# Kernel tuning notes

Hardware: AMD Instinct MI355X
Metric: run time of the kernel (lower is better)

Reference implementation:

```python
import jax, jax.numpy as jnp
import numpy as np
from jax import lax

DIM = 256
HEADS = 8
DIM_HEAD = 64
INNER = HEADS * DIM_HEAD  # 512
K = 3
PAD = K // 2
KV_STRIDE = 2
SCALE = DIM_HEAD ** -0.5
BN_EPS = 1e-5


def _dw_block(x, w_dw, g, b, m, v, w_pw, stride):
    """depthwise conv -> batchnorm (eval) -> 1x1 conv. x: [B,C,H,W]."""
    c = x.shape[1]
    h = lax.conv_general_dilated(
        x, w_dw, window_strides=(stride, stride),
        padding=[(PAD, PAD), (PAD, PAD)],
        feature_group_count=c,
        dimension_numbers=('NCHW', 'OIHW', 'NCHW'))
    inv = lax.rsqrt(v + BN_EPS)
    h = (h - m[None, :, None, None]) * (g * inv)[None, :, None, None] + b[None, :, None, None]
    return jnp.einsum('oc,bchw->bohw', w_pw, h)


def _heads_flat(t):
    # [B, h*d, H, W] -> [B, h, d, H*W]
    B, hd, H, W = t.shape
    return t.reshape(B, HEADS, DIM_HEAD, H * W)


def _cross_attn(q, k, v, Hq, Wq):
    # q: [B,h,d,i], k/v: [B,h,d,j]
    dots = jnp.einsum('bhdi,bhdj->bhij', q, k) * SCALE
    attn = jax.nn.softmax(dots, axis=-1)
    out = jnp.einsum('bhij,bhdj->bhdi', attn, v)
    B = q.shape[0]
    return out.reshape(B, INNER, Hq, Wq)


def _forward(x, y, q_dw_w, q_bn_gamma, q_bn_beta, q_bn_mean, q_bn_var, q_pw_w,
             kv_dw_w, kv_bn_gamma, kv_bn_beta, kv_bn_mean, kv_bn_var, kv_pw_w,
             out_w, out_b):
    B, _, Hx, Wx = x.shape
    _, _, Hy, Wy = y.shape

    qx = _heads_flat(_dw_block(x, q_dw_w, q_bn_gamma, q_bn_beta, q_bn_mean, q_bn_var, q_pw_w, 1))
    kvx = _dw_block(x, kv_dw_w, kv_bn_gamma, kv_bn_beta, kv_bn_mean, kv_bn_var, kv_pw_w, KV_STRIDE)
    kx, vx = map(_heads_flat, jnp.split(kvx, 2, axis=1))

    qy = _heads_flat(_dw_block(y, q_dw_w, q_bn_gamma, q_bn_beta, q_bn_mean, q_bn_var, q_pw_w, 1))
    kvy = _dw_block(y, kv_dw_w, kv_bn_gamma, kv_bn_beta, kv_bn_mean, kv_bn_var, kv_pw_w, KV_STRIDE)
    ky, vy = map(_heads_flat, jnp.split(kvy, 2, axis=1))

    outx = _cross_attn(qx, ky, vy, Hx, Wx)   # x queries attend to y keys/values
    outy = _cross_attn(qy, kx, vx, Hy, Wy)   # y queries attend to x keys/values

    def proj(o):
        return jnp.einsum('oc,bchw->bohw', out_w, o) + out_b[None, :, None, None]

    return proj(outx), proj(outy)


def setup_inputs() -> dict:
    key = jax.random.key(0)
    ks = jax.random.split(key, 8)
    B, H, W = 8, 32, 32
    return {
        'x': jax.random.normal(ks[0], (B, DIM, H, W), jnp.float32),
        'y': jax.random.normal(ks[1], (B, DIM, H, W), jnp.float32),
        'q_dw_w': jax.random.normal(ks[2], (DIM, 1, K, K), jnp.float32) * 0.1,
        'q_bn_gamma': jnp.ones((DIM,), jnp.float32),
        'q_bn_beta': jnp.zeros((DIM,), jnp.float32),
        'q_bn_mean': jnp.zeros((DIM,), jnp.float32),
        'q_bn_var': jnp.ones((DIM,), jnp.float32),
        'q_pw_w': jax.random.normal(ks[3], (INNER, DIM), jnp.float32) * (DIM ** -0.5),
        'kv_dw_w': jax.random.normal(ks[4], (DIM, 1, K, K), jnp.float32) * 0.1,
        'kv_bn_gamma': jnp.ones((DIM,), jnp.float32),
        'kv_bn_beta': jnp.zeros((DIM,), jnp.float32),
        'kv_bn_mean': jnp.zeros((DIM,), jnp.float32),
        'kv_bn_var': jnp.ones((DIM,), jnp.float32),
        'kv_pw_w': jax.random.normal(ks[5], (2 * INNER, DIM), jnp.float32) * (DIM ** -0.5),
        'out_w': jax.random.normal(ks[6], (DIM, INNER), jnp.float32) * (INNER ** -0.5),
        'out_b': jnp.zeros((DIM,), jnp.float32),
    }


def reference(x, y, q_dw_w, q_bn_gamma, q_bn_beta, q_bn_mean, q_bn_var, q_pw_w,
              kv_dw_w, kv_bn_gamma, kv_bn_beta, kv_bn_mean, kv_bn_var, kv_pw_w,
              out_w, out_b):
    return _forward(x, y, q_dw_w, q_bn_gamma, q_bn_beta, q_bn_mean, q_bn_var, q_pw_w,
                    kv_dw_w, kv_bn_gamma, kv_bn_beta, kv_bn_mean, kv_bn_var, kv_pw_w,
                    out_w, out_b)
```

## Files before the change

### kernel.cpp

```cpp
#include <hip/hip_runtime.h>

#define BN_EPS 1e-5f
#define ATT_SCALE 0.125f

typedef _Float16 half_t;
typedef _Float16 half8 __attribute__((ext_vector_type(8)));
typedef _Float16 half4 __attribute__((ext_vector_type(4)));
typedef float f32x4 __attribute__((ext_vector_type(4)));

__device__ __forceinline__ void gll16(const void* g, void* l) {
    __builtin_amdgcn_global_load_lds((const __attribute__((address_space(1))) void*)g,
                                     (__attribute__((address_space(3))) void*)l, 16, 0, 0);
}

__device__ void prep_body(
    int o, int c,
    const float* qg, const float* qb, const float* qm, const float* qv, const float* qpw,
    const float* kg, const float* kbt, const float* km, const float* kvv, const float* kvpw,
    const float* outw,
    half_t* wq, half_t* wkv, half_t* wout, float* bq, float* bkv, float* red)
{
    if (o >= 1536) {
        int ro = o - 1536;
        #pragma unroll
        for (int ci = 0; ci < 2; ++ci) {
            int cc = ci * 256 + c;
            float wv = outw[(size_t)ro * 512 + cc];
            half_t hh = (half_t)wv;
            wout[(size_t)ro * 1024 + cc]       = hh;
            wout[(size_t)ro * 1024 + 512 + cc] = (half_t)(wv - (float)hh);
        }
        return;
    }
    const float *g, *b, *m, *v, *w; half_t* we; float* be;
    if (o < 512) {
        g = qg; b = qb; m = qm; v = qv;
        w = qpw + (size_t)o * 256; we = wq + (size_t)o * 512; be = bq + o;
    } else {
        int ro = o - 512;
        g = kg; b = kbt; m = km; v = kvv;
        w = kvpw + (size_t)ro * 256; we = wkv + (size_t)ro * 512; be = bkv + ro;
    }
    float s  = g[c] * rsqrtf(v[c] + BN_EPS);
    float tt = b[c] - m[c] * s;
    float wv = w[c];
    float wsv = wv * s;
    half_t hh = (half_t)wsv;
    we[c]       = hh;
    we[256 + c] = (half_t)(wsv - (float)hh);
    float partial = wv * tt;
    #pragma unroll
    for (int off = 32; off > 0; off >>= 1)
        partial += __shfl_down(partial, off, 64);
    if ((c & 63) == 0) red[c >> 6] = partial;
    __syncthreads();
    if (c == 0) *be = red[0] + red[1] + red[2] + red[3];
}

__device__ void dw_body(
    int rp, int img, float* sin,
    const float* x, const float* y,
    const float* qdw, const float* kvdw,
    half_t* qB, half_t* kvB)
{
    const float* in = (img < 8) ? x + (size_t)img * 256 * 1024
// ... 37 lines not shown
            #pragma unroll
            for (int c8 = 0; c8 < 8; ++c8) {
                float acc = 0.f;
                #pragma unroll
                for (int dr = 0; dr < 3; ++dr)
                    #pragma unroll
                    for (int dc = 0; dc < 3; ++dc)
                        acc += wq9[dr * 3 + dc] * rowv[r + dr][c8 + dc + 1];
                half_t hh = (half_t)acc;
                size_t p = (size_t)img * 1024 + (2 * rp + r) * 32 + cg * 8 + c8;
                qB[p * 512 + gch]       = hh;
                qB[p * 512 + 256 + gch] = (half_t)(acc - (float)hh);
            }
        }
        #pragma unroll
        for (int c4 = 0; c4 < 4; ++c4) {
            float acc = 0.f;
            #pragma unroll
            for (int dr = 0; dr < 3; ++dr)
                #pragma unroll
                for (int dc = 0; dc < 3; ++dc)
                    acc += wk9[dr * 3 + dc] * rowv[dr][2 * c4 + dc + 1];
            half_t hh = (half_t)acc;
            size_t p = (size_t)img * 256 + rp * 16 + cg * 4 + c4;
            kvB[p * 512 + gch]       = hh;
            kvB[p * 512 + 256 + gch] = (half_t)(acc - (float)hh);
        }
    }
}

__global__ __launch_bounds__(256) void prep_dw_kernel(
    const float* __restrict__ x, const float* __restrict__ y,
    const float* __restrict__ qdw, const float* __restrict__ kvdw,
    const float* __restrict__ qg, const float* __restrict__ qb,
    const float* __restrict__ qm, const float* __restrict__ qv,
    const float* __restrict__ qpw,
    const float* __restrict__ kg, const float* __restrict__ kbt,
    const float* __restrict__ km, const float* __restrict__ kvv,
    const float* __restrict__ kvpw,
    const float* __restrict__ outw,
    half_t* __restrict__ wq, half_t* __restrict__ wkv, half_t* __restrict__ wout,
    float* __restrict__ bq, float* __restrict__ bkv,
    half_t* __restrict__ qB, half_t* __restrict__ kvB)
{
    __shared__ __align__(16) float smem[64 * 148];
    int bx = blockIdx.x;
    if (bx < 256)
        dw_body(bx & 15, bx >> 4, smem, x, y, qdw, kvdw, qB, kvB);
    else
        prep_body(bx - 256, threadIdx.x, qg, qb, qm, qv, qpw,
                  kg, kbt, km, kvv, kvpw, outw, wq, wkv, wout, bq, bkv, smem);
}

template<int MT, int NT, int WGM, int WGN, int NTHR, int MODE>
__device__ __forceinline__ void gemm_worker(
    char* lds, const half_t* Ab, const half_t* Bb,
    void* outBuf, const float* bias,
    int K, int NPX, int img, int m0, int n0, float scale)
{
    constexpr int TM = WGM * MT * 16, TN = WGN * NT * 16;
    constexpr int BUF = (TM + TN) * 128;
    int t = threadIdx.x, w = t >> 6, lane = t & 63, quad = lane >> 4, l15 = lane & 15;
    int wm = w % WGM, wn = w / WGM;
    f32x4 acc[MT][NT] = {};
    const int NC = K / 32;

    auto stage = [&](int kh, int p) {
        char* Ah = lds + p * BUF;
        char* Al = Ah + TM * 64;
        char* Bh = Ah + TM * 128;
        char* Bl = Bh + TN * 64;
        #pragma unroll
        for (int ii = 0; ii < TM * 4 / NTHR; ++ii) {
            int u = ii * NTHR + t;
            int mt = u >> 6, q = (u >> 4) & 3, r = u & 15;
            const half_t* g = Ab + (size_t)(mt * 16 + r) * (2 * K) + kh + q * 8;
            gll16(g,     Ah + (u & ~63) * 16);
            gll16(g + K, Al + (u & ~63) * 16);
        }
        #pragma unroll
        for (int ii = 0; ii < TN * 4 / NTHR; ++ii) {
            int u = ii * NTHR + t;
            int nt = u >> 6, q = (u >> 4) & 3, r = u & 15;
            const half_t* g = Bb + (size_t)(nt * 16 + r) * (2 * K) + kh + q * 8;
            gll16(g,     Bh + (u & ~63) * 16);
            gll16(g + K, Bl + (u & ~63) * 16);
        }
    };

    stage(0, 0);
    for (int kc = 0; kc < NC; ++kc) {
        __syncthreads();
        if (kc + 1 < NC) stage((kc + 1) * 32, (kc + 1) & 1);
        char* Ah = lds + (kc & 1) * BUF;
        char* Al = Ah + TM * 64;
        char* Bh = Ah + TM * 128;
        char* Bl = Bh + TN * 64;
        half8 afh[MT], afl[MT];
        #pragma unroll
        for (int mi = 0; mi < MT; ++mi) {
            afh[mi] = *(half8*)(Ah + (wm * MT + mi) * 1024 + lane * 16);
            afl[mi] = *(half8*)(Al + (wm * MT + mi) * 1024 + lane * 16);
        }
        #pragma unroll
        for (int ni = 0; ni < NT; ++ni) {
            half8 bh = *(half8*)(Bh + (wn * NT + ni) * 1024 + lane * 16);
            half8 bl = *(half8*)(Bl + (wn * NT + ni) * 1024 + lane * 16);
            #pragma unroll
            for (int mi = 0; mi < MT; ++mi) {
                acc[mi][ni] = __builtin_amdgcn_mfma_f32_16x16x32_f16(afh[mi], bh, acc[mi][ni], 0, 0, 0);
                acc[mi][ni] = __builtin_amdgcn_mfma_f32_16x16x32_f16(afh[mi], bl, acc[mi][ni], 0, 0, 0);
                acc[mi][ni] = __builtin_amdgcn_mfma_f32_16x16x32_f16(afl[mi], bh, acc[mi][ni], 0, 0, 0);
            }
        }
    }

    if (MODE == 2) {
        #pragma unroll
        for (int mi = 0; mi < MT; ++mi) {
            int mrow0 = m0 + wm * MT * 16 + mi * 16 + quad * 4;
            #pragma unroll
            for (int ni = 0; ni < NT; ++ni) {
                int col = n0 + wn * NT * 16 + ni * 16 + l15;
                f32x4 a = acc[mi][ni];
                float* op = (float*)outBuf + (size_t)img * 256 * NPX;
                #pragma unroll
                for (int r = 0; r < 4; ++r)
                    op[(size_t)(mrow0 + r) * NPX + col] = a[r] + bias[mrow0 + r];
            }
        }
    } else {
        __syncthreads();
        float* tbuf = (float*)lds;
        constexpr int TP = 40;
        #pragma unroll
        for (int qtr = 0; qtr < TM / 32; ++qtr) {
            #pragma unroll
            for (int mi = 0; mi < MT; ++mi) {
                int rowblk = wm * MT * 16 + mi * 16;
                if (rowblk >= qtr * 32 && rowblk < qtr * 32 + 32) {
                    int mloc = rowblk - qtr * 32 + quad * 4;
                    #pragma unroll
                    for (int ni = 0; ni < NT; ++ni) {
                        int nloc = wn * NT * 16 + ni * 16 + l15;
                        #pragma unroll
                        for (int r = 0; r < 4; ++r) {
                            float vv = acc[mi][ni][r];
                            if (MODE == 0) vv = (vv + bias[m0 + rowblk + quad * 4 + r]) * scale;
                            else           vv = vv + bias[n0 + nloc];
                            tbuf[nloc * TP + mloc + r] = vv;
                        }
                    }
                }
            }
            __syncthreads();
            #pragma unroll
            for (int it = 0; it < (TN * 4) / NTHR; ++it) {
                int u = it * NTHR + t;
                int n = u >> 2, mg = u & 3;
                float vv[8];
                *(float4*)&vv[0] = *(const float4*)&tbuf[n * TP + mg * 8];
                *(float4*)&vv[4] = *(const float4*)&tbuf[n * TP + mg * 8 + 4];
                half8 hv, lv;
                #pragma unroll
                for (int j = 0; j < 8; ++j) {
                    half_t hh = (half_t)vv[j];
                    hv[j] = hh; lv[j] = (half_t)(vv[j] - (float)hh);
                }
                int mglob = m0 + qtr * 32 + mg * 8;
                if (MODE == 0) {
                    int h = mglob >> 6, d0 = mglob & 63;
                    half_t* op = (half_t*)outBuf + ((size_t)(img * 8 + h) * NPX + n0 + n) * 128 + d0;
                    *(half8*)op = hv;
                    *(half8*)(op + 64) = lv;
                } else {
                    int nn = n0 + n, h = nn >> 6, d = nn & 63;
                    int j0 = mglob;
                    half_t* op = (half_t*)outBuf + (size_t)(img * 8 + h) * 32768
                               + (j0 >> 5) * 4096 + ((d >> 4) & 3) * 512 + ((j0 >> 4) & 1) * 256
                               + ((j0 >> 2) & 3) * 64 + (d & 15) * 4;
                    half4 a0 = {hv[0], hv[1], hv[2], hv[3]};
                    half4 a1 = {hv[4], hv[5], hv[6], hv[7]};
                    half4 b0 = {lv[0], lv[1], lv[2], lv[3]};
                    half4 b1 = {lv[4], lv[5], lv[6], lv[7]};
                    *(half4*)op               = a0;
                    *(half4*)(op + 64)        = a1;
                    *(half4*)(op + 2048)      = b0;
                    *(half4*)(op + 2048 + 64) = b1;
                }
            }
            __syncthreads();
        }
    }
}

__global__ __launch_bounds__(512, 4) void qkv_kernel(
    const half_t* __restrict__ wq, const half_t* __restrict__ wkv,
    const half_t* __restrict__ qB, const half_t* __restrict__ kvB,
    const float* __restrict__ bq, const float* __restrict__ bkv,
    half_t* __restrict__ qpr, half_t* __restrict__ kpr, half_t* __restrict__ vpr)
{
    __shared__ __align__(16) char lds[65536];
    int tile = blockIdx.x, img = blockIdx.z;
    if (tile < 32) {
        int m0 = (tile >> 3) * 128, n0 = (tile & 7) * 128;
        gemm_worker<2, 4, 4, 2, 512, 0>(lds,
            wq + (size_t)m0 * 512,
            qB + (size_t)img * (1024 * 512) + (size_t)n0 * 512,
            qpr, bq, 256, 1024, img, m0, n0, ATT_SCALE);
    } else if (tile < 40) {
        int tt = tile - 32;
        int m0 = (tt >> 1) * 128, n0 = (tt & 1) * 128;
        gemm_worker<2, 4, 4, 2, 512, 0>(lds,
            wkv + (size_t)m0 * 512,
            kvB + (size_t)img * (256 * 512) + (size_t)n0 * 512,
            kpr, bkv, 256, 256, img, m0, n0, 1.0f);
    } else {
        int tt = tile - 40;
        int m0 = (tt >> 2) * 128, n0 = (tt & 3) * 128;
        gemm_worker<2, 4, 4, 2, 512, 1>(lds,
            kvB + (size_t)img * (256 * 512) + (size_t)m0 * 512,
            wkv + (size_t)(512 + n0) * 512,
            vpr, bkv + 512, 256, 512, img, m0, n0, 1.0f);
    }
}

__global__ __launch_bounds__(256, 3) void out_kernel(
    const half_t* __restrict__ wout, const half_t* __restrict__ attp,
    const float* __restrict__ outb, float* __restrict__ out)
{
    __shared__ __align__(16) char lds[49152];
    int tile = blockIdx.x, img = blockIdx.z;
    int m0 = (tile >> 3) * 64, n0 = (tile & 7) * 128;
    gemm_worker<2, 4, 2, 2, 256, 2>(lds,
        wout + (size_t)m0 * 1024,
        attp + (size_t)img * (1024 * 1024) + (size_t)n0 * 1024,
        out, outb, 512, 1024, img, m0, n0, 1.0f);
}

__global__ __launch_bounds__(256, 4) void attn_fused(
    const half_t* __restrict__ qb, const half_t* __restrict__ kb,
    const half_t* __restrict__ vb, half_t* __restrict__ att)
{
    __shared__ __align__(16) char lds[17408];
    int ic2 = blockIdx.y;
    int img = blockIdx.x & 15, h = blockIdx.x >> 4;
    int partner = img ^ 8;
    int t = threadIdx.x, w = t >> 6, lane = t & 63, quad = lane >> 4, l15 = lane & 15;
    const half_t* qp = qb + ((size_t)(img * 8 + h) * 1024 + ic2 * 64) * 128;
    const half_t* kp = kb + (size_t)(partner * 8 + h) * 256 * 128;
    const half_t* vp = vb + (size_t)(partner * 8 + h) * 32768;

    half8 qh[2], ql[2];
    #pragma unroll
    for (int kcs = 0; kcs < 2; ++kcs) {
        const half_t* qr = qp + (size_t)(w * 16 + l15) * 128 + kcs * 32 + quad * 8;
        qh[kcs] = *(const half8*)qr;
        ql[kcs] = *(const half8*)(qr + 64);
    }

    auto stageK = [&](int c, char* buf) {
        #pragma unroll
        for (int s = 0; s < 2; ++s) {
            int u = s * 256 + t;
            int sb = u >> 6, li = u & 63;
            int plane = sb >> 2, ntr = (sb >> 1) & 1, kcs = sb & 1;
            const half_t* g = kp + (size_t)(c * 32 + ntr * 16 + (li & 15)) * 128
                                 + plane * 64 + kcs * 32 + (li >> 4) * 8;
            gll16(g, buf + (u & ~63) * 16);
        }
    };
    auto stageV = [&](int c, char* buf) {
        #pragma unroll
        for (int s = 0; s < 2; ++s) {
            int u = s * 256 + t;
            gll16(vp + (size_t)c * 4096 + u * 8, buf + (u & ~63) * 16);
        }
    };

    f32x4 sacc[16] = {};
    stageK(0, lds);
    #pragma unroll
    for (int c = 0; c < 8; ++c) {
        __syncthreads();
        char* nb = lds + (((c + 1) & 1) * 8192);
        if (c < 7) stageK(c + 1, nb); else stageV(0, nb);
        const char* buf = lds + ((c & 1) * 8192);
        __builtin_amdgcn_s_setprio(1);
        #pragma unroll
        for (int kcs = 0; kcs < 2; ++kcs)
            #pragma unroll
            for (int ntr = 0; ntr < 2; ++ntr) {
                half8 kh = *(const half8*)(buf + (ntr * 2 + kcs) * 1024 + lane * 16);
                half8 kl = *(const half8*)(buf + 4096 + (ntr * 2 + kcs) * 1024 + lane * 16);
                f32x4 s = sacc[c * 2 + ntr];
                s = __builtin_amdgcn_mfma_f32_16x16x32_f16(kh, qh[kcs], s, 0, 0, 0);
                s = __builtin_amdgcn_mfma_f32_16x16x32_f16(kh, ql[kcs], s, 0, 0, 0);
                s = __builtin_amdgcn_mfma_f32_16x16x32_f16(kl, qh[kcs], s, 0, 0, 0);
                sacc[c * 2 + ntr] = s;
            }
        __builtin_amdgcn_s_setprio(0);
    }

    float mx = sacc[0][0];
    #pragma unroll
    for (int ti = 0; ti < 16; ++ti)
        #pragma unroll
        for (int r = 0; r < 4; ++r) mx = fmaxf(mx, sacc[ti][r]);
    mx = fmaxf(mx, __shfl_xor(mx, 16, 64));
    mx = fmaxf(mx, __shfl_xor(mx, 32, 64));

    f32x4 oacc[4] = {};
    float lsum = 0.f;
    #pragma unroll
    for (int c = 0; c < 8; ++c) {
        half4 pb[2][2];
        #pragma unroll
        for (int kk = 0; kk < 2; ++kk) {
            f32x4 s = sacc[c * 2 + kk];
            #pragma unroll
            for (int e = 0; e < 4; ++e) {
                float pv = __expf(s[e] - mx);
                lsum += pv;
                half_t hh = (half_t)pv;
                pb[kk][0][e] = hh;
                pb[kk][1][e] = (half_t)(pv - (float)hh);
            }
        }
        __syncthreads();
        if (c < 7) stageV(c + 1, lds + (((c + 1) & 1) * 8192));
        const char* buf = lds + ((c & 1) * 8192);
        __builtin_amdgcn_s_setprio(1);
        #pragma unroll
        for (int mt = 0; mt < 4; ++mt) {
            #pragma unroll
            for (int kk = 0; kk < 2; ++kk) {
                half4 vh = *(const half4*)(buf + (mt * 2 + kk) * 512 + lane * 8);
                half4 vl = *(const half4*)(buf + 4096 + (mt * 2 + kk) * 512 + lane * 8);
                f32x4 o = oacc[mt];
                o = __builtin_amdgcn_mfma_f32_16x16x16f16(vh, pb[kk][0], o, 0, 0, 0);
                o = __builtin_amdgcn_mfma_f32_16x16x16f16(vh, pb[kk][1], o, 0, 0, 0);
                o = __builtin_amdgcn_mfma_f32_16x16x16f16(vl, pb[kk][0], o, 0, 0, 0);
                oacc[mt] = o;
            }
        }
        __builtin_amdgcn_s_setprio(0);
    }

    lsum += __shfl_xor(lsum, 16, 64);
    lsum += __shfl_xor(lsum, 32, 64);
    float inv = 1.f / lsum;

    __syncthreads();
    #pragma unroll
    for (int mt = 0; mt < 4; ++mt)
        #pragma unroll
        for (int r = 0; r < 4; ++r) {
            float vv = oacc[mt][r] * inv;
            half_t hh = (half_t)vv;
            int row = w * 16 + l15;
            int d = mt * 16 + quad * 4 + r;
            *(half_t*)(lds + (row * 132 + d) * 2)      = hh;
            *(half_t*)(lds + (row * 132 + 64 + d) * 2) = (half_t)(vv - (float)hh);
        }
    __syncthreads();
    #pragma unroll
    for (int ii = 0; ii < 4; ++ii) {
        int u = ii * 256 + t;
        int i = u >> 4, s16 = u & 15;
        half8 val = *(const half8*)(lds + (i * 132 + (s16 >> 3) * 64 + (s16 & 7) * 8) * 2);
        *(half8*)(att + ((size_t)img * 1024 + ic2 * 64 + i) * 1024
                  + (s16 >> 3) * 512 + h * 64 + (s16 & 7) * 8) = val;
    }
}

extern "C" void kernel_launch(void* const* d_in, const int* in_sizes, int n_in,
                              void* d_out, int out_size, void* d_ws, size_t ws_size,
                              hipStream_t stream) {
    const float* x    = (const float*)d_in[0];
    const float* y    = (const float*)d_in[1];
    const float* qdw  = (const float*)d_in[2];
    const float* qg   = (const float*)d_in[3];
    const float* qbb  = (const float*)d_in[4];
    const float* qm   = (const float*)d_in[5];
    const float* qv   = (const float*)d_in[6];
    const float* qpw  = (const float*)d_in[7];
    const float* kvdw = (const float*)d_in[8];
    const float* kg   = (const float*)d_in[9];
    const float* kb_  = (const float*)d_in[10];
    const float* km   = (const float*)d_in[11];
    const float* kvv  = (const float*)d_in[12];
    const float* kvpw = (const float*)d_in[13];
    const float* outw = (const float*)d_in[14];
    const float* outb = (const float*)d_in[15];

    char* ws = (char*)d_ws;
    half_t* wq   = (half_t*)(ws);
    half_t* wkv  = (half_t*)(ws + 524288);
    half_t* wout = (half_t*)(ws + 1572864);
    float*  bq   = (float*) (ws + 2097152);
    float*  bkv  = (float*) (ws + 2099200);
    half_t* qpr  = (half_t*)(ws + 2103296);
    half_t* kpr  = (half_t*)(ws + 35657728);
    half_t* vpr  = (half_t*)(ws + 44046336);
    half_t* qB   = (half_t*)(ws + 52434944);
    half_t* kvB  = (half_t*)(ws + 69212160);
    half_t* attp = (half_t*)(ws + 52434944);

    prep_dw_kernel<<<2048, 256, 0, stream>>>(
        x, y, qdw, kvdw, qg, qbb, qm, qv, qpw, kg, kb_, km, kvv, kvpw, outw,
        wq, wkv, wout, bq, bkv, qB, kvB);

    qkv_kernel<<<dim3(48, 1, 16), 512, 0, stream>>>(
        wq, wkv, qB, kvB, bq, bkv, qpr, kpr, vpr);

    attn_fused<<<dim3(128, 16, 1), 256, 0, stream>>>(qpr, kpr, vpr, attp);

    out_kernel<<<dim3(32, 1, 16), 256, 0, stream>>>(wout, attp, outb, (float*)d_out);
}
```

Baseline: 213.3 us.

## Use 256x256 register-staged QKV tiles and deeper-pipelined 128-query attention blocks

Measured after the change: 219.0 us. +2.7%, slower.

```diff
diff --git a/kernel.cpp b/kernel.cpp
--- a/kernel.cpp
+++ b/kernel.cpp
@@ -11,6 +11,11 @@
 __device__ __forceinline__ void gll16(const void* g, void* l) {
     __builtin_amdgcn_global_load_lds((const __attribute__((address_space(1))) void*)g,
                                      (__attribute__((address_space(3))) void*)l, 16, 0, 0);
+}
+
+template<int N>
+__device__ __forceinline__ void vmwait() {
+    asm volatile("s_waitcnt vmcnt(%0)" :: "i"(N) : "memory");
 }
 
 __device__ void prep_body(
@@ -154,6 +159,172 @@
                   kg, kbt, km, kvv, kvpw, outw, wq, wkv, wout, bq, bkv, smem);
 }
 
+template<int MODE>
+__device__ void gemm_sq(char* lds, const half_t* Ab, const half_t* Bb,
+                        void* outBuf, const float* bias,
+                        int NPX, int img, int m0, int n0, float scale)
+{
+    int t = threadIdx.x, w = t >> 6, lane = t & 63, quad = lane >> 4, l15 = lane & 15;
+    int wm = w & 3, wn = w >> 2;
+    f32x4 acc[4][4] = {};
+
+    const int side = t >> 9, pl = (t >> 8) & 1, r = t & 255;
+    const half_t* gsrc = (side ? Bb : Ab) + (size_t)r * 512 + pl * 256;
+    char* ldst = lds + side * 32768 + pl * 16384 + r * 16;
+
+    half8 greg[4];
+    #pragma unroll
+    for (int q = 0; q < 4; ++q) greg[q] = *(const half8*)(gsrc + q * 8);
+
+    for (int kc = 0; kc < 8; ++kc) {
+        __syncthreads();
+        #pragma unroll
+        for (int q = 0; q < 4; ++q) *(half8*)(ldst + q * 4096) = greg[q];
+        __syncthreads();
+        if (kc < 7) {
+            const half_t* gs2 = gsrc + (kc + 1) * 32;
+            #pragma unroll
+            for (int q = 0; q < 4; ++q) greg[q] = *(const half8*)(gs2 + q * 8);
+        }
+        #pragma unroll
+        for (int mh = 0; mh < 2; ++mh) {
+            half8 mfh[2], mfl[2];
+            #pragma unroll
+            for (int mi2 = 0; mi2 < 2; ++mi2) {
+                int mrow = (wm * 4 + mh * 2 + mi2) * 16 + l15;
+                mfh[mi2] = *(const half8*)(lds + quad * 4096 + mrow * 16);
+                mfl[mi2] = *(const half8*)(lds + 16384 + quad * 4096 + mrow * 16);
+            }
+            #pragma unroll
+            for (int ni = 0; ni < 4; ++ni) {
+                int nrow = (wn * 4 + ni) * 16 + l15;
+                half8 nh = *(const half8*)(lds + 32768 + quad * 4096 + nrow * 16);
+                half8 nl = *(const half8*)(lds + 49152 + quad * 4096 + nrow * 16);
+                #pragma unroll
+                for (int mi2 = 0; mi2 < 2; ++mi2) {
+                    int mi = mh * 2 + mi2;
+                    acc[mi][ni] = __builtin_amdgcn_mfma_f32_16x16x32_f16(mfh[mi2], nh, acc[mi][ni], 0, 0, 0);
+                    acc[mi][ni] = __builtin_amdgcn_mfma_f32_16x16x32_f16(mfh[mi2], nl, acc[mi][ni], 0, 0, 0);
+                    acc[mi][ni] = __builtin_amdgcn_mfma_f32_16x16x32_f16(mfl[mi2], nh, acc[mi][ni], 0, 0, 0);
+                }
+            }
+        }
+    }
+
+    if (MODE == 0) {
+        float* tbuf = (float*)lds;
+        #pragma unroll
+        for (int rr = 0; rr < 8; ++rr) {
+            __syncthreads();
+            if (wm == (rr >> 1)) {
+                #pragma unroll
+                for (int mi2 = 0; mi2 < 2; ++mi2) {
+                    int mi = (rr & 1) * 2 + mi2;
+                    #pragma unroll
+                    for (int ni = 0; ni < 4; ++ni)
+                        #pragma unroll
+                        for (int r4 = 0; r4 < 4; ++r4) {
+                            float vv = (acc[mi][ni][r4]
+                                        + bias[m0 + rr * 32 + mi2 * 16 + quad * 4 + r4]) * scale;
+                            tbuf[(wn * 64 + ni * 16 + l15) * 36 + mi2 * 16 + quad * 4 + r4] = vv;
+                        }
+                }
+            }
+            __syncthreads();
+            {
+                int n = t >> 2, mg = t & 3;
+                float vv[8];
+                *(float4*)&vv[0] = *(const float4*)&tbuf[n * 36 + mg * 8];
+                *(float4*)&vv[4] = *(const float4*)&tbuf[n * 36 + mg * 8 + 4];
+                half8 hv, lv;
+                #pragma unroll
+                for (int j = 0; j < 8; ++j) {
+                    half_t hh = (half_t)vv[j];
+                    hv[j] = hh; lv[j] = (half_t)(vv[j] - (float)hh);
+                }
+                int mglob = m0 + rr * 32 + mg * 8;
+                int h = mglob >> 6, d0 = mglob & 63;
+                half_t* op = (half_t*)outBuf + ((size_t)(img * 8 + h) * NPX + n0 + n) * 128 + d0;
+                *(half8*)op = hv;
+                *(half8*)(op + 64) = lv;
+            }
+        }
+    } else {
+        float* tbuf = (float*)lds;
+        constexpr int TP = 40;
+        #pragma unroll
+        for (int qtr = 0; qtr < 8; ++qtr) {
+            __syncthreads();
+            if (wm == (qtr >> 1)) {
+                #pragma unroll
+                for (int mi2 = 0; mi2 < 2; ++mi2) {
+                    int mi = (qtr & 1) * 2 + mi2;
+                    #pragma unroll
+                    for (int ni = 0; ni < 4; ++ni) {
+                        int nloc = wn * 64 + ni * 16 + l15;
+                        #pragma unroll
+                        for (int r4 = 0; r4 < 4; ++r4)
+                            tbuf[nloc * TP + mi2 * 16 + quad * 4 + r4] =
+                                acc[mi][ni][r4] + bias[n0 + nloc];
+                    }
+                }
+            }
+            __syncthreads();
+            {
+                int n = t >> 2, mg = t & 3;
+                float vv[8];
+                *(float4*)&vv[0] = *(const float4*)&tbuf[n * TP + mg * 8];
+                *(float4*)&vv[4] = *(const float4*)&tbuf[n * TP + mg * 8 + 4];
+                half8 hv, lv;
+                #pragma unroll
+                for (int j = 0; j < 8; ++j) {
+                    half_t hh = (half_t)vv[j];
+                    hv[j] = hh; lv[j] = (half_t)(vv[j] - (float)hh);
+                }
+                int j0 = qtr * 32 + mg * 8;
+                int nn = n0 + n, h = nn >> 6, d = nn & 63;
+                half_t* op = (half_t*)outBuf + (size_t)(img * 8 + h) * 32768
+                           + (j0 >> 5) * 4096 + ((d >> 4) & 3) * 512 + ((j0 >> 4) & 1) * 256
+                           + ((j0 >> 2) & 3) * 64 + (d & 15) * 4;
+                half4 a0 = {hv[0], hv[1], hv[2], hv[3]};
+                half4 a1 = {hv[4], hv[5], hv[6], hv[7]};
+                half4 b0 = {lv[0], lv[1], lv[2], lv[3]};
+                half4 b1 = {lv[4], lv[5], lv[6], lv[7]};
+                *(half4*)op               = a0;
+                *(half4*)(op + 64)        = a1;
+                *(half4*)(op + 2048)      = b0;
+                *(half4*)(op + 2048 + 64) = b1;
+            }
+        }
+    }
+}
+
+__global__ __launch_bounds__(1024, 4) void qkv_kernel(
+    const half_t* __restrict__ wq, const half_t* __restrict__ wkv,
+    const half_t* __restrict__ qB, const half_t* __restrict__ kvB,
+    const float* __restrict__ bq, const float* __restrict__ bkv,
+    half_t* __restrict__ qpr, half_t* __restrict__ kpr, half_t* __restrict__ vpr)
+{
+    __shared__ __align__(16) char lds[65536];
+    int tile = blockIdx.x, img = blockIdx.z;
+    if (tile < 8) {
+        int m0 = (tile >> 2) * 256, n0 = (tile & 3) * 256;
+        gemm_sq<0>(lds, wq + (size_t)m0 * 512,
+                   qB + (size_t)img * (1024 * 512) + (size_t)n0 * 512,
+                   qpr, bq, 1024, img, m0, n0, ATT_SCALE);
+    } else if (tile < 10) {
+        int m0 = (tile - 8) * 256;
+        gemm_sq<0>(lds, wkv + (size_t)m0 * 512,
+                   kvB + (size_t)img * (256 * 512),
+                   kpr, bkv, 256, img, m0, 0, 1.0f);
+    } else {
+        int n0 = (tile - 10) * 256;
+        gemm_sq<1>(lds, kvB + (size_t)img * (256 * 512),
+                   wkv + (size_t)(512 + n0) * 512,
+                   vpr, bkv + 512, 512, img, 0, n0, 1.0f);
+    }
+}
+
 template<int MT, int NT, int WGM, int WGN, int NTHR, int MODE>
 __device__ __forceinline__ void gemm_worker(
     char* lds, const half_t* Ab, const half_t* Bb,
@@ -175,16 +346,16 @@
         #pragma unroll
         for (int ii = 0; ii < TM * 4 / NTHR; ++ii) {
             int u = ii * NTHR + t;
-            int mt = u >> 6, q = (u >> 4) & 3, r = u & 15;
-            const half_t* g = Ab + (size_t)(mt * 16 + r) * (2 * K) + kh + q * 8;
+            int mt = u >> 6, q = (u >> 4) & 3, rr = u & 15;
+            const half_t* g = Ab + (size_t)(mt * 16 + rr) * (2 * K) + kh + q * 8;
             gll16(g,     Ah + (u & ~63) * 16);
             gll16(g + K, Al + (u & ~63) * 16);
         }
         #pragma unroll
         for (int ii = 0; ii < TN * 4 / NTHR; ++ii) {
             int u = ii * NTHR + t;
-            int nt = u >> 6, q = (u >> 4) & 3, r = u & 15;
-            const half_t* g = Bb + (size_t)(nt * 16 + r) * (2 * K) + kh + q * 8;
+            int nt = u >> 6, q = (u >> 4) & 3, rr = u & 15;
+            const half_t* g = Bb + (size_t)(nt * 16 + rr) * (2 * K) + kh + q * 8;
             gll16(g,     Bh + (u & ~63) * 16);
             gll16(g + K, Bl + (u & ~63) * 16);
         }
@@ -217,113 +388,18 @@
         }
     }
 
-    if (MODE == 2) {
-        #pragma unroll
-        for (int mi = 0; mi < MT; ++mi) {
-            int mrow0 = m0 + wm * MT * 16 + mi * 16 + quad * 4;
-            #pragma unroll
-            for (int ni = 0; ni < NT; ++ni) {
-                int col = n0 + wn * NT * 16 + ni * 16 + l15;
-                f32x4 a = acc[mi][ni];
-                float* op = (float*)outBuf + (size_t)img * 256 * NPX;
-                #pragma unroll
-                for (int r = 0; r < 4; ++r)
-                    op[(size_t)(mrow0 + r) * NPX + col] = a[r] + bias[mrow0 + r];
-            }
-        }
-    } else {
-        __syncthreads();
-        float* tbuf = (float*)lds;
-        constexpr int TP = 40;
-        #pragma unroll
-        for (int qtr = 0; qtr < TM / 32; ++qtr) {
-            #pragma unroll
-            for (int mi = 0; mi < MT; ++mi) {
-                int rowblk = wm * MT * 16 + mi * 16;
-                if (rowblk >= qtr * 32 && rowblk < qtr * 32 + 32) {
-                    int mloc = rowblk - qtr * 32 + quad * 4;
-                    #pragma unroll
-                    for (int ni = 0; ni < NT; ++ni) {
-                        int nloc = wn * NT * 16 + ni * 16 + l15;
-                        #pragma unroll
-                        for (int r = 0; r < 4; ++r) {
-                            float vv = acc[mi][ni][r];
-                            if (MODE == 0) vv = (vv + bias[m0 + rowblk + quad * 4 + r]) * scale;
-                            else           vv = vv + bias[n0 + nloc];
-                            tbuf[nloc * TP + mloc + r] = vv;
-                        }
-                    }
-                }
-            }
-            __syncthreads();
-            #pragma unroll
-            for (int it = 0; it < (TN * 4) / NTHR; ++it) {
-                int u = it * NTHR + t;
-                int n = u >> 2, mg = u & 3;
-                float vv[8];
-                *(float4*)&vv[0] = *(const float4*)&tbuf[n * TP + mg * 8];
-                *(float4*)&vv[4] = *(const float4*)&tbuf[n * TP + mg * 8 + 4];
-                half8 hv, lv;
-                #pragma unroll
-                for (int j = 0; j < 8; ++j) {
-                    half_t hh = (half_t)vv[j];
-                    hv[j] = hh; lv[j] = (half_t)(vv[j] - (float)hh);
-                }
-                int mglob = m0 + qtr * 32 + mg * 8;
-                if (MODE == 0) {
-                    int h = mglob >> 6, d0 = mglob & 63;
-                    half_t* op = (half_t*)outBuf + ((size_t)(img * 8 + h) * NPX + n0 + n) * 128 + d0;
-                    *(half8*)op = hv;
-                    *(half8*)(op + 64) = lv;
-                } else {
-                    int nn = n0 + n, h = nn >> 6, d = nn & 63;
-                    int j0 = mglob;
-                    half_t* op = (half_t*)outBuf + (size_t)(img * 8 + h) * 32768
-                               + (j0 >> 5) * 4096 + ((d >> 4) & 3) * 512 + ((j0 >> 4) & 1) * 256
-                               + ((j0 >> 2) & 3) * 64 + (d & 15) * 4;
-                    half4 a0 = {hv[0], hv[1], hv[2], hv[3]};
-                    half4 a1 = {hv[4], hv[5], hv[6], hv[7]};
-                    half4 b0 = {lv[0], lv[1], lv[2], lv[3]};
-                    half4 b1 = {lv[4], lv[5], lv[6], lv[7]};
-                    *(half4*)op               = a0;
-                    *(half4*)(op + 64)        = a1;
-                    *(half4*)(op + 2048)      = b0;
-                    *(half4*)(op + 2048 + 64) = b1;
-                }
-            }
-            __syncthreads();
-        }
-    }
-}
-
-__global__ __launch_bounds__(512, 4) void qkv_kernel(
-    const half_t* __restrict__ wq, const half_t* __restrict__ wkv,
-    const half_t* __restrict__ qB, const half_t* __restrict__ kvB,
-    const float* __restrict__ bq, const float* __restrict__ bkv,
-    half_t* __restrict__ qpr, half_t* __restrict__ kpr, half_t* __restrict__ vpr)
-{
-    __shared__ __align__(16) char lds[65536];
-    int tile = blockIdx.x, img = blockIdx.z;
-    if (tile < 32) {
-        int m0 = (tile >> 3) * 128, n0 = (tile & 7) * 128;
-        gemm_worker<2, 4, 4, 2, 512, 0>(lds,
-            wq + (size_t)m0 * 512,
-            qB + (size_t)img * (1024 * 512) + (size_t)n0 * 512,
-            qpr, bq, 256, 1024, img, m0, n0, ATT_SCALE);
-    } else if (tile < 40) {
-        int tt = tile - 32;
-        int m0 = (tt >> 1) * 128, n0 = (tt & 1) * 128;
-        gemm_worker<2, 4, 4, 2, 512, 0>(lds,
-            wkv + (size_t)m0 * 512,
-            kvB + (size_t)img * (256 * 512) + (size_t)n0 * 512,
-            kpr, bkv, 256, 256, img, m0, n0, 1.0f);
-    } else {
-        int tt = tile - 40;
-        int m0 = (tt >> 2) * 128, n0 = (tt & 3) * 128;
-        gemm_worker<2, 4, 4, 2, 512, 1>(lds,
-            kvB + (size_t)img * (256 * 512) + (size_t)m0 * 512,
-            wkv + (size_t)(512 + n0) * 512,
-            vpr, bkv + 512, 256, 512, img, m0, n0, 1.0f);
+    #pragma unroll
+    for (int mi = 0; mi < MT; ++mi) {
+        int mrow0 = m0 + wm * MT * 16 + mi * 16 + quad * 4;
+        #pragma unroll
+        for (int ni = 0; ni < NT; ++ni) {
+            int col = n0 + wn * NT * 16 + ni * 16 + l15;
+            f32x4 a = acc[mi][ni];
+            float* op = (float*)outBuf + (size_t)img * 256 * NPX;
+            #pragma unroll
+            for (int rr = 0; rr < 4; ++rr)
+                op[(size_t)(mrow0 + rr) * NPX + col] = a[rr] + bias[mrow0 + rr];
+        }
     }
 }
 
@@ -340,16 +416,16 @@
         out, outb, 512, 1024, img, m0, n0, 1.0f);
 }
 
-__global__ __launch_bounds__(256, 4) void attn_fused(
+__global__ __launch_bounds__(512, 4) void attn_fused(
     const half_t* __restrict__ qb, const half_t* __restrict__ kb,
     const half_t* __restrict__ vb, half_t* __restrict__ att)
 {
-    __shared__ __align__(16) char lds[17408];
-    int ic2 = blockIdx.y;
+    __shared__ __align__(16) char lds[33792];
+    int ic = blockIdx.y;
     int img = blockIdx.x & 15, h = blockIdx.x >> 4;
     int partner = img ^ 8;
     int t = threadIdx.x, w = t >> 6, lane = t & 63, quad = lane >> 4, l15 = lane & 15;
-    const half_t* qp = qb + ((size_t)(img * 8 + h) * 1024 + ic2 * 64) * 128;
+    const half_t* qp = qb + ((size_t)(img * 8 + h) * 1024 + ic * 128) * 128;
     const half_t* kp = kb + (size_t)(partner * 8 + h) * 256 * 128;
     const half_t* vp = vb + (size_t)(partner * 8 + h) * 32768;
 
@@ -361,92 +437,89 @@
         ql[kcs] = *(const half8*)(qr + 64);
     }
 
-    auto stageK = [&](int c, char* buf) {
-        #pragma unroll
-        for (int s = 0; s < 2; ++s) {
-            int u = s * 256 + t;
-            int sb = u >> 6, li = u & 63;
+    auto stageC = [&](int c) {
+        char* buf = lds + (c & 3) * 8192;
+        if (c < 8) {
+            int sb = t >> 6, li = t & 63;
             int plane = sb >> 2, ntr = (sb >> 1) & 1, kcs = sb & 1;
             const half_t* g = kp + (size_t)(c * 32 + ntr * 16 + (li & 15)) * 128
                                  + plane * 64 + kcs * 32 + (li >> 4) * 8;
-            gll16(g, buf + (u & ~63) * 16);
+            gll16(g, buf + (t & ~63) * 16);
+        } else {
+            gll16(vp + (size_t)(c - 8) * 4096 + t * 8, buf + (t & ~63) * 16);
         }
     };
-    auto stageV = [&](int c, char* buf) {
-        #pragma unroll
-        for (int s = 0; s < 2; ++s) {
-            int u = s * 256 + t;
-            gll16(vp + (size_t)c * 4096 + u * 8, buf + (u & ~63) * 16);
-        }
-    };
 
     f32x4 sacc[16] = {};
-    stageK(0, lds);
-    #pragma unroll
-    for (int c = 0; c < 8; ++c) {
-        __syncthreads();
-        char* nb = lds + (((c + 1) & 1) * 8192);
-        if (c < 7) stageK(c + 1, nb); else stageV(0, nb);
-        const char* buf = lds + ((c & 1) * 8192);
-        __builtin_amdgcn_s_setprio(1);
-        #pragma unroll
-        for (int kcs = 0; kcs < 2; ++kcs)
-            #pragma unroll
-            for (int ntr = 0; ntr < 2; ++ntr) {
-                half8 kh = *(const half8*)(buf + (ntr * 2 + kcs) * 1024 + lane * 16);
-                half8 kl = *(const half8*)(buf + 4096 + (ntr * 2 + kcs) * 1024 + lane * 16);
-                f32x4 s = sacc[c * 2 + ntr];
-                s = __builtin_amdgcn_mfma_f32_16x16x32_f16(kh, qh[kcs], s, 0, 0, 0);
-                s = __builtin_amdgcn_mfma_f32_16x16x32_f16(kh, ql[kcs], s, 0, 0, 0);
-                s = __builtin_amdgcn_mfma_f32_16x16x32_f16(kl, qh[kcs], s, 0, 0, 0);
-                sacc[c * 2 + ntr] = s;
-            }
-        __builtin_amdgcn_s_setprio(0);
-    }
-
-    float mx = sacc[0][0];
-    #pragma unroll
-    for (int ti = 0; ti < 16; ++ti)
-        #pragma unroll
-        for (int r = 0; r < 4; ++r) mx = fmaxf(mx, sacc[ti][r]);
-    mx = fmaxf(mx, __shfl_xor(mx, 16, 64));
-    mx = fmaxf(mx, __shfl_xor(mx, 32, 64));
-
     f32x4 oacc[4] = {};
-    float lsum = 0.f;
-    #pragma unroll
-    for (int c = 0; c < 8; ++c) {
-        half4 pb[2][2];
-        #pragma unroll
-        for (int kk = 0; kk < 2; ++kk) {
-            f32x4 s = sacc[c * 2 + kk];
-            #pragma unroll
-            for (int e = 0; e < 4; ++e) {
-                float pv = __expf(s[e] - mx);
-                lsum += pv;
-                half_t hh = (half_t)pv;
-                pb[kk][0][e] = hh;
-                pb[kk][1][e] = (half_t)(pv - (float)hh);
-            }
-        }
-        __syncthreads();
-        if (c < 7) stageV(c + 1, lds + (((c + 1) & 1) * 8192));
-        const char* buf = lds + ((c & 1) * 8192);
-        __builtin_amdgcn_s_setprio(1);
-        #pragma unroll
-        for (int mt = 0; mt < 4; ++mt) {
+    float mx = 0.f, lsum = 0.f;
+
+    stageC(0); stageC(1); stageC(2);
+
+    #pragma unroll
+    for (int c = 0; c < 16; ++c) {
+        if (c < 14)       vmwait<2>();
+        else if (c == 14) vmwait<1>();
+        else              vmwait<0>();
+        __builtin_amdgcn_s_barrier();
+        __builtin_amdgcn_sched_barrier(0);
+        if (c + 3 < 16) stageC(c + 3);
+        const char* buf = lds + (c & 3) * 8192;
+        if (c < 8) {
+            __builtin_amdgcn_s_setprio(1);
+            #pragma unroll
+            for (int kcs = 0; kcs < 2; ++kcs)
+                #pragma unroll
+                for (int ntr = 0; ntr < 2; ++ntr) {
+                    half8 kh = *(const half8*)(buf + (ntr * 2 + kcs) * 1024 + lane * 16);
+                    half8 kl = *(const half8*)(buf + 4096 + (ntr * 2 + kcs) * 1024 + lane * 16);
+                    f32x4 s = sacc[c * 2 + ntr];
+                    s = __builtin_amdgcn_mfma_f32_16x16x32_f16(kh, qh[kcs], s, 0, 0, 0);
+                    s = __builtin_amdgcn_mfma_f32_16x16x32_f16(kh, ql[kcs], s, 0, 0, 0);
+                    s = __builtin_amdgcn_mfma_f32_16x16x32_f16(kl, qh[kcs], s, 0, 0, 0);
+                    sacc[c * 2 + ntr] = s;
+                }
+            __builtin_amdgcn_s_setprio(0);
+        } else {
+            if (c == 8) {
+                float m_ = sacc[0][0];
+                #pragma unroll
+                for (int ti = 0; ti < 16; ++ti)
+                    #pragma unroll
+                    for (int r = 0; r < 4; ++r) m_ = fmaxf(m_, sacc[ti][r]);
+                m_ = fmaxf(m_, __shfl_xor(m_, 16, 64));
+                mx = fmaxf(m_, __shfl_xor(m_, 32, 64));
+            }
+            int jc = c - 8;
+            half4 pb[2][2];
             #pragma unroll
             for (int kk = 0; kk < 2; ++kk) {
-                half4 vh = *(const half4*)(buf + (mt * 2 + kk) * 512 + lane * 8);
-                half4 vl = *(const half4*)(buf + 4096 + (mt * 2 + kk) * 512 + lane * 8);
-                f32x4 o = oacc[mt];
-                o = __builtin_amdgcn_mfma_f32_16x16x16f16(vh, pb[kk][0], o, 0, 0, 0);
-                o = __builtin_amdgcn_mfma_f32_16x16x16f16(vh, pb[kk][1], o, 0, 0, 0);
-                o = __builtin_amdgcn_mfma_f32_16x16x16f16(vl, pb[kk][0], o, 0, 0, 0);
-                oacc[mt] = o;
-            }
-        }
-        __builtin_amdgcn_s_setprio(0);
+                f32x4 s = sacc[jc * 2 + kk];
+                #pragma unroll
+                for (int e = 0; e < 4; ++e) {
+                    float pv = __expf(s[e] - mx);
+                    lsum += pv;
+                    half_t hh = (half_t)pv;
+                    pb[kk][0][e] = hh;
+                    pb[kk][1][e] = (half_t)(pv - (float)hh);
+                }
+            }
+            __builtin_amdgcn_s_setprio(1);
+            #pragma unroll
+            for (int mt = 0; mt < 4; ++mt) {
+                #pragma unroll
+                for (int kk = 0; kk < 2; ++kk) {
+                    half4 vh = *(const half4*)(buf + (mt * 2 + kk) * 512 + lane * 8);
+                    half4 vl = *(const half4*)(buf + 4096 + (mt * 2 + kk) * 512 + lane * 8);
+                    f32x4 o = oacc[mt];
+                    o = __builtin_amdgcn_mfma_f32_16x16x16f16(vh, pb[kk][0], o, 0, 0, 0);
+                    o = __builtin_amdgcn_mfma_f32_16x16x16f16(vh, pb[kk][1], o, 0, 0, 0);
+                    o = __builtin_amdgcn_mfma_f32_16x16x16f16(vl, pb[kk][0], o, 0, 0, 0);
+                    oacc[mt] = o;
+                }
+            }
+            __builtin_amdgcn_s_setprio(0);
+        }
     }
 
     lsum += __shfl_xor(lsum, 16, 64);
@@ -468,11 +541,11 @@
     __syncthreads();
     #pragma unroll
     for (int ii = 0; ii < 4; ++ii) {
-        int u = ii * 256 + t;
-        int i = u >> 4, s16 = u & 15;
-        half8 val = *(const half8*)(lds + (i * 132 + (s16 >> 3) * 64 + (s16 & 7) * 8) * 2);
-        *(half8*)(att + ((size_t)img * 1024 + ic2 * 64 + i) * 1024
-                  + (s16 >> 3) * 512 + h * 64 + (s16 & 7) * 8) = val;
+        int u = ii * 512 + t;
+        int i = u >> 4, seg = (u >> 3) & 1, p8 = u & 7;
+        half8 val = *(const half8*)(lds + (i * 132 + seg * 64 + p8 * 8) * 2);
+        *(half8*)(att + ((size_t)img * 1024 + ic * 128 + i) * 1024
+                  + seg * 512 + h * 64 + p8 * 8) = val;
     }
 }
 
@@ -513,10 +586,10 @@
         x, y, qdw, kvdw, qg, qbb, qm, qv, qpw, kg, kb_, km, kvv, kvpw, outw,
         wq, wkv, wout, bq, bkv, qB, kvB);
 
-    qkv_kernel<<<dim3(48, 1, 16), 512, 0, stream>>>(
+    qkv_kernel<<<dim3(12, 1, 16), 1024, 0, stream>>>(
         wq, wkv, qB, kvB, bq, bkv, qpr, kpr, vpr);
 
-    attn_fused<<<dim3(128, 16, 1), 256, 0, stream>>>(qpr, kpr, vpr, attp);
+    attn_fused<<<dim3(128, 8, 1), 512, 0, stream>>>(qpr, kpr, vpr, attp);
 
     out_kernel<<<dim3(32, 1, 16), 256, 0, stream>>>(wout, attp, outb, (float*)d_out);
 }
```

## Deepen attention pipeline, widen blocks, and use vmcnt-based barriers in GEMM

Applied to the files above, without the earlier changes.

Result: faster. 204.0 us (-4.4%).

```diff
diff --git a/kernel.cpp b/kernel.cpp
--- a/kernel.cpp
+++ b/kernel.cpp
@@ -11,6 +11,11 @@
 __device__ __forceinline__ void gll16(const void* g, void* l) {
     __builtin_amdgcn_global_load_lds((const __attribute__((address_space(1))) void*)g,
                                      (__attribute__((address_space(3))) void*)l, 16, 0, 0);
+}
+
+template<int N>
+__device__ __forceinline__ void vmwait() {
+    asm volatile("s_waitcnt vmcnt(%0)" :: "i"(N) : "memory");
 }
 
 __device__ void prep_body(
@@ -154,18 +159,19 @@
                   kg, kbt, km, kvv, kvpw, outw, wq, wkv, wout, bq, bkv, smem);
 }
 
-template<int MT, int NT, int WGM, int WGN, int NTHR, int MODE>
+template<int MT, int NT, int WGM, int WGN, int NTHR, int MODE, int KTOT>
 __device__ __forceinline__ void gemm_worker(
     char* lds, const half_t* Ab, const half_t* Bb,
     void* outBuf, const float* bias,
-    int K, int NPX, int img, int m0, int n0, float scale)
+    int NPX, int img, int m0, int n0, float scale)
 {
     constexpr int TM = WGM * MT * 16, TN = WGN * NT * 16;
     constexpr int BUF = (TM + TN) * 128;
+    constexpr int NC = KTOT / 32;
+    constexpr int GCNT = 8 * (TM + TN) / NTHR;
     int t = threadIdx.x, w = t >> 6, lane = t & 63, quad = lane >> 4, l15 = lane & 15;
     int wm = w % WGM, wn = w / WGM;
     f32x4 acc[MT][NT] = {};
-    const int NC = K / 32;
 
     auto stage = [&](int kh, int p) {
         char* Ah = lds + p * BUF;
@@ -176,24 +182,26 @@
         for (int ii = 0; ii < TM * 4 / NTHR; ++ii) {
             int u = ii * NTHR + t;
             int mt = u >> 6, q = (u >> 4) & 3, r = u & 15;
-            const half_t* g = Ab + (size_t)(mt * 16 + r) * (2 * K) + kh + q * 8;
-            gll16(g,     Ah + (u & ~63) * 16);
-            gll16(g + K, Al + (u & ~63) * 16);
+            const half_t* g = Ab + (size_t)(mt * 16 + r) * (2 * KTOT) + kh + q * 8;
+            gll16(g,        Ah + (u & ~63) * 16);
+            gll16(g + KTOT, Al + (u & ~63) * 16);
         }
         #pragma unroll
         for (int ii = 0; ii < TN * 4 / NTHR; ++ii) {
             int u = ii * NTHR + t;
             int nt = u >> 6, q = (u >> 4) & 3, r = u & 15;
-            const half_t* g = Bb + (size_t)(nt * 16 + r) * (2 * K) + kh + q * 8;
-            gll16(g,     Bh + (u & ~63) * 16);
-            gll16(g + K, Bl + (u & ~63) * 16);
+            const half_t* g = Bb + (size_t)(nt * 16 + r) * (2 * KTOT) + kh + q * 8;
+            gll16(g,        Bh + (u & ~63) * 16);
+            gll16(g + KTOT, Bl + (u & ~63) * 16);
         }
     };
 
     stage(0, 0);
     for (int kc = 0; kc < NC; ++kc) {
-        __syncthreads();
-        if (kc + 1 < NC) stage((kc + 1) * 32, (kc + 1) & 1);
+        if (kc + 1 < NC) { stage((kc + 1) * 32, (kc + 1) & 1); vmwait<GCNT>(); }
+        else             { vmwait<0>(); }
+        __builtin_amdgcn_s_barrier();
+        __builtin_amdgcn_sched_barrier(0);
         char* Ah = lds + (kc & 1) * BUF;
         char* Al = Ah + TM * 64;
         char* Bh = Ah + TM * 128;
@@ -204,6 +212,7 @@
             afh[mi] = *(half8*)(Ah + (wm * MT + mi) * 1024 + lane * 16);
             afl[mi] = *(half8*)(Al + (wm * MT + mi) * 1024 + lane * 16);
         }
+        __builtin_amdgcn_s_setprio(1);
         #pragma unroll
         for (int ni = 0; ni < NT; ++ni) {
             half8 bh = *(half8*)(Bh + (wn * NT + ni) * 1024 + lane * 16);
@@ -215,6 +224,9 @@
                 acc[mi][ni] = __builtin_amdgcn_mfma_f32_16x16x32_f16(afl[mi], bh, acc[mi][ni], 0, 0, 0);
             }
         }
+        __builtin_amdgcn_s_setprio(0);
+        __builtin_amdgcn_s_barrier();
+        __builtin_amdgcn_sched_barrier(0);
     }
 
     if (MODE == 2) {
@@ -306,24 +318,24 @@
     int tile = blockIdx.x, img = blockIdx.z;
     if (tile < 32) {
         int m0 = (tile >> 3) * 128, n0 = (tile & 7) * 128;
-        gemm_worker<2, 4, 4, 2, 512, 0>(lds,
+        gemm_worker<2, 4, 4, 2, 512, 0, 256>(lds,
             wq + (size_t)m0 * 512,
             qB + (size_t)img * (1024 * 512) + (size_t)n0 * 512,
-            qpr, bq, 256, 1024, img, m0, n0, ATT_SCALE);
+            qpr, bq, 1024, img, m0, n0, ATT_SCALE);
     } else if (tile < 40) {
         int tt = tile - 32;
         int m0 = (tt >> 1) * 128, n0 = (tt & 1) * 128;
-        gemm_worker<2, 4, 4, 2, 512, 0>(lds,
+        gemm_worker<2, 4, 4, 2, 512, 0, 256>(lds,
             wkv + (size_t)m0 * 512,
             kvB + (size_t)img * (256 * 512) + (size_t)n0 * 512,
-            kpr, bkv, 256, 256, img, m0, n0, 1.0f);
+            kpr, bkv, 256, img, m0, n0, 1.0f);
     } else {
         int tt = tile - 40;
         int m0 = (tt >> 2) * 128, n0 = (tt & 3) * 128;
-        gemm_worker<2, 4, 4, 2, 512, 1>(lds,
+        gemm_worker<2, 4, 4, 2, 512, 1, 256>(lds,
             kvB + (size_t)img * (256 * 512) + (size_t)m0 * 512,
             wkv + (size_t)(512 + n0) * 512,
-            vpr, bkv + 512, 256, 512, img, m0, n0, 1.0f);
+            vpr, bkv + 512, 512, img, m0, n0, 1.0f);
     }
 }
 
@@ -334,22 +346,22 @@
     __shared__ __align__(16) char lds[49152];
     int tile = blockIdx.x, img = blockIdx.z;
     int m0 = (tile >> 3) * 64, n0 = (tile & 7) * 128;
-    gemm_worker<2, 4, 2, 2, 256, 2>(lds,
+    gemm_worker<2, 4, 2, 2, 256, 2, 512>(lds,
         wout + (size_t)m0 * 1024,
         attp + (size_t)img * (1024 * 1024) + (size_t)n0 * 1024,
-        out, outb, 512, 1024, img, m0, n0, 1.0f);
-}
-
-__global__ __launch_bounds__(256, 4) void attn_fused(
+        out, outb, 1024, img, m0, n0, 1.0f);
+}
+
+__global__ __launch_bounds__(512, 4) void attn_fused(
     const half_t* __restrict__ qb, const half_t* __restrict__ kb,
     const half_t* __restrict__ vb, half_t* __restrict__ att)
 {
-    __shared__ __align__(16) char lds[17408];
-    int ic2 = blockIdx.y;
+    __shared__ __align__(16) char lds[33792];
+    int ic = blockIdx.y;
     int img = blockIdx.x & 15, h = blockIdx.x >> 4;
     int partner = img ^ 8;
     int t = threadIdx.x, w = t >> 6, lane = t & 63, quad = lane >> 4, l15 = lane & 15;
-    const half_t* qp = qb + ((size_t)(img * 8 + h) * 1024 + ic2 * 64) * 128;
+    const half_t* qp = qb + ((size_t)(img * 8 + h) * 1024 + ic * 128) * 128;
     const half_t* kp = kb + (size_t)(partner * 8 + h) * 256 * 128;
     const half_t* vp = vb + (size_t)(partner * 8 + h) * 32768;
 
@@ -361,92 +373,89 @@
         ql[kcs] = *(const half8*)(qr + 64);
     }
 
-    auto stageK = [&](int c, char* buf) {
-        #pragma unroll
-        for (int s = 0; s < 2; ++s) {
-            int u = s * 256 + t;
-            int sb = u >> 6, li = u & 63;
+    auto stageC = [&](int c) {
+        char* buf = lds + (c & 3) * 8192;
+        if (c < 8) {
+            int sb = t >> 6, li = t & 63;
             int plane = sb >> 2, ntr = (sb >> 1) & 1, kcs = sb & 1;
             const half_t* g = kp + (size_t)(c * 32 + ntr * 16 + (li & 15)) * 128
                                  + plane * 64 + kcs * 32 + (li >> 4) * 8;
-            gll16(g, buf + (u & ~63) * 16);
+            gll16(g, buf + (t & ~63) * 16);
+        } else {
+            gll16(vp + (size_t)(c - 8) * 4096 + t * 8, buf + (t & ~63) * 16);
         }
     };
-    auto stageV = [&](int c, char* buf) {
-        #pragma unroll
-        for (int s = 0; s < 2; ++s) {
-            int u = s * 256 + t;
-            gll16(vp + (size_t)c * 4096 + u * 8, buf + (u & ~63) * 16);
-        }
-    };
 
     f32x4 sacc[16] = {};
-    stageK(0, lds);
+    f32x4 oacc[4] = {};
+    float mx = 0.f, lsum = 0.f;
+
+    stageC(0); stageC(1); stageC(2);
+
     #pragma unroll
-    for (int c = 0; c < 8; ++c) {
-        __syncthreads();
-        char* nb = lds + (((c + 1) & 1) * 8192);
-        if (c < 7) stageK(c + 1, nb); else stageV(0, nb);
-        const char* buf = lds + ((c & 1) * 8192);
-        __builtin_amdgcn_s_setprio(1);
-        #pragma unroll
-        for (int kcs = 0; kcs < 2; ++kcs)
-            #pragma unroll
-            for (int ntr = 0; ntr < 2; ++ntr) {
-                half8 kh = *(const half8*)(buf + (ntr * 2 + kcs) * 1024 + lane * 16);
-                half8 kl = *(const half8*)(buf + 4096 + (ntr * 2 + kcs) * 1024 + lane * 16);
-                f32x4 s = sacc[c * 2 + ntr];
-                s = __builtin_amdgcn_mfma_f32_16x16x32_f16(kh, qh[kcs], s, 0, 0, 0);
-                s = __builtin_amdgcn_mfma_f32_16x16x32_f16(kh, ql[kcs], s, 0, 0, 0);
-                s = __builtin_amdgcn_mfma_f32_16x16x32_f16(kl, qh[kcs], s, 0, 0, 0);
-                sacc[c * 2 + ntr] = s;
-            }
-        __builtin_amdgcn_s_setprio(0);
-    }
-
-    float mx = sacc[0][0];
-    #pragma unroll
-    for (int ti = 0; ti < 16; ++ti)
-        #pragma unroll
-        for (int r = 0; r < 4; ++r) mx = fmaxf(mx, sacc[ti][r]);
-    mx = fmaxf(mx, __shfl_xor(mx, 16, 64));
-    mx = fmaxf(mx, __shfl_xor(mx, 32, 64));
-
-    f32x4 oacc[4] = {};
-    float lsum = 0.f;
-    #pragma unroll
-    for (int c = 0; c < 8; ++c) {
-        half4 pb[2][2];
-        #pragma unroll
-        for (int kk = 0; kk < 2; ++kk) {
-            f32x4 s = sacc[c * 2 + kk];
-            #pragma unroll
-            for (int e = 0; e < 4; ++e) {
-                float pv = __expf(s[e] - mx);
-                lsum += pv;
-                half_t hh = (half_t)pv;
-                pb[kk][0][e] = hh;
-                pb[kk][1][e] = (half_t)(pv - (float)hh);
-            }
-        }
-        __syncthreads();
-        if (c < 7) stageV(c + 1, lds + (((c + 1) & 1) * 8192));
-        const char* buf = lds + ((c & 1) * 8192);
-        __builtin_amdgcn_s_setprio(1);
-        #pragma unroll
-        for (int mt = 0; mt < 4; ++mt) {
+    for (int c = 0; c < 16; ++c) {
+        if (c < 14)       vmwait<2>();
+        else if (c == 14) vmwait<1>();
+        else              vmwait<0>();
+        __builtin_amdgcn_s_barrier();
+        __builtin_amdgcn_sched_barrier(0);
+        if (c + 3 < 16) stageC(c + 3);
+        const char* buf = lds + (c & 3) * 8192;
+        if (c < 8) {
+            __builtin_amdgcn_s_setprio(1);
+            #pragma unroll
+            for (int kcs = 0; kcs < 2; ++kcs)
+                #pragma unroll
+                for (int ntr = 0; ntr < 2; ++ntr) {
+                    half8 kh = *(const half8*)(buf + (ntr * 2 + kcs) * 1024 + lane * 16);
+                    half8 kl = *(const half8*)(buf + 4096 + (ntr * 2 + kcs) * 1024 + lane * 16);
+                    f32x4 s = sacc[c * 2 + ntr];
+                    s = __builtin_amdgcn_mfma_f32_16x16x32_f16(kh, qh[kcs], s, 0, 0, 0);
+                    s = __builtin_amdgcn_mfma_f32_16x16x32_f16(kh, ql[kcs], s, 0, 0, 0);
+                    s = __builtin_amdgcn_mfma_f32_16x16x32_f16(kl, qh[kcs], s, 0, 0, 0);
+                    sacc[c * 2 + ntr] = s;
+                }
+            __builtin_amdgcn_s_setprio(0);
+        } else {
+            if (c == 8) {
+                float m_ = sacc[0][0];
+                #pragma unroll
+                for (int ti = 0; ti < 16; ++ti)
+                    #pragma unroll
+                    for (int r = 0; r < 4; ++r) m_ = fmaxf(m_, sacc[ti][r]);
+                m_ = fmaxf(m_, __shfl_xor(m_, 16, 64));
+                mx = fmaxf(m_, __shfl_xor(m_, 32, 64));
+            }
+            int jc = c - 8;
+            half4 pb[2][2];
             #pragma unroll
             for (int kk = 0; kk < 2; ++kk) {
-                half4 vh = *(const half4*)(buf + (mt * 2 + kk) * 512 + lane * 8);
-                half4 vl = *(const half4*)(buf + 4096 + (mt * 2 + kk) * 512 + lane * 8);
-                f32x4 o = oacc[mt];
-                o = __builtin_amdgcn_mfma_f32_16x16x16f16(vh, pb[kk][0], o, 0, 0, 0);
-                o = __builtin_amdgcn_mfma_f32_16x16x16f16(vh, pb[kk][1], o, 0, 0, 0);
-                o = __builtin_amdgcn_mfma_f32_16x16x16f16(vl, pb[kk][0], o, 0, 0, 0);
-                oacc[mt] = o;
-            }
-        }
-        __builtin_amdgcn_s_setprio(0);
+                f32x4 s = sacc[jc * 2 + kk];
+                #pragma unroll
+                for (int e = 0; e < 4; ++e) {
+                    float pv = __expf(s[e] - mx);
+                    lsum += pv;
+                    half_t hh = (half_t)pv;
+                    pb[kk][0][e] = hh;
+                    pb[kk][1][e] = (half_t)(pv - (float)hh);
+                }
+            }
+            __builtin_amdgcn_s_setprio(1);
+            #pragma unroll
+            for (int mt = 0; mt < 4; ++mt) {
+                #pragma unroll
+                for (int kk = 0; kk < 2; ++kk) {
+                    half4 vh = *(const half4*)(buf + (mt * 2 + kk) * 512 + lane * 8);
+                    half4 vl = *(const half4*)(buf + 4096 + (mt * 2 + kk) * 512 + lane * 8);
+                    f32x4 o = oacc[mt];
+                    o = __builtin_amdgcn_mfma_f32_16x16x16f16(vh, pb[kk][0], o, 0, 0, 0);
+                    o = __builtin_amdgcn_mfma_f32_16x16x16f16(vh, pb[kk][1], o, 0, 0, 0);
+                    o = __builtin_amdgcn_mfma_f32_16x16x16f16(vl, pb[kk][0], o, 0, 0, 0);
+                    oacc[mt] = o;
+                }
+            }
+            __builtin_amdgcn_s_setprio(0);
+        }
     }
 
     lsum += __shfl_xor(lsum, 16, 64);
@@ -468,11 +477,11 @@
     __syncthreads();
     #pragma unroll
     for (int ii = 0; ii < 4; ++ii) {
-        int u = ii * 256 + t;
-        int i = u >> 4, s16 = u & 15;
-        half8 val = *(const half8*)(lds + (i * 132 + (s16 >> 3) * 64 + (s16 & 7) * 8) * 2);
-        *(half8*)(att + ((size_t)img * 1024 + ic2 * 64 + i) * 1024
-                  + (s16 >> 3) * 512 + h * 64 + (s16 & 7) * 8) = val;
+        int u = ii * 512 + t;
+        int i = u >> 4, seg = (u >> 3) & 1, p8 = u & 7;
+        half8 val = *(const half8*)(lds + (i * 132 + seg * 64 + p8 * 8) * 2);
+        *(half8*)(att + ((size_t)img * 1024 + ic * 128 + i) * 1024
+                  + seg * 512 + h * 64 + p8 * 8) = val;
     }
 }
 
@@ -516,7 +525,7 @@
     qkv_kernel<<<dim3(48, 1, 16), 512, 0, stream>>>(
         wq, wkv, qB, kvB, bq, bkv, qpr, kpr, vpr);
 
-    attn_fused<<<dim3(128, 16, 1), 256, 0, stream>>>(qpr, kpr, vpr, attp);
+    attn_fused<<<dim3(128, 8, 1), 512, 0, stream>>>(qpr, kpr, vpr, attp);
 
     out_kernel<<<dim3(32, 1, 16), 256, 0, stream>>>(wout, attp, outb, (float*)d_out);
 }
```
